# Optimization experiments

Hardware: AMD Instinct MI355X
Metric: run time of the kernel (lower is better)

## Reference

```python
import jax, jax.numpy as jnp
import numpy as np

N_USERS = 100000
M_ITEMS = 50000
EMBED = 64
N_LAYERS = 3
NNZ = 2400000
BATCH = 8192


def setup_inputs() -> dict:
    key = jax.random.key(0)
    ks = jax.random.split(key, 8)
    user = jax.random.randint(ks[0], (BATCH,), 0, N_USERS)
    item_i = jax.random.randint(ks[1], (BATCH,), 0, M_ITEMS)
    item_j = jax.random.randint(ks[2], (BATCH,), 0, M_ITEMS)
    timestamp = jax.random.uniform(ks[3], (BATCH,), dtype=jnp.float32)
    # symmetric bipartite edge list: user->item and item->user halves
    half = NNZ // 2
    u = jax.random.randint(ks[4], (half,), 0, N_USERS)
    it = jax.random.randint(ks[5], (half,), 0, M_ITEMS) + N_USERS
    edge_src = jnp.concatenate([u, it])
    edge_dst = jnp.concatenate([it, u])
    v = jax.random.uniform(ks[6], (half,), dtype=jnp.float32)
    edge_vals = jnp.concatenate([v, v])  # symmetric normalized weights
    embed_user_0 = jax.random.normal(ks[7], (N_USERS, EMBED), dtype=jnp.float32) * 0.1
    embed_item_0 = jax.random.normal(jax.random.fold_in(key, 99), (M_ITEMS, EMBED), dtype=jnp.float32) * 0.1
    return {
        'user': user, 'item_i': item_i, 'item_j': item_j,
        'timestamp': timestamp, 'split_idx': 0,
        'edge_src': edge_src, 'edge_dst': edge_dst, 'edge_vals': edge_vals,
        'embed_user_0': embed_user_0, 'embed_item_0': embed_item_0,
    }


def reference(user, item_i, item_j, timestamp, split_idx,
              edge_src, edge_dst, edge_vals, embed_user_0, embed_item_0):
    N = N_USERS + M_ITEMS
    # LightGCN propagation: mean over layer-0..n_layers embeddings
    all_emb = jnp.concatenate([embed_user_0, embed_item_0], axis=0)  # [N, D]
    emb = all_emb
    emb_sum = all_emb
    for _ in range(N_LAYERS):
        # sparse.mm(Graph, emb): gather source features along edges, scale, segment-reduce
        emb = jax.ops.segment_sum(edge_vals[:, None] * emb[edge_dst], edge_src,
                                  num_segments=N)
        emb_sum = emb_sum + emb
    light_out = emb_sum / (N_LAYERS + 1)
    embed_user = light_out[:N_USERS]
    embed_item = light_out[N_USERS:]

    ue = embed_user[user]          # [B, D]
    ie = embed_item[item_i]        # [B, D]
    je = embed_item[item_j]        # [B, D]
    prediction_i = jnp.sum(ue * ie, axis=-1)
    prediction_j = jnp.sum(ue * je, axis=-1)

    # reg_loss uses layer-0 embeddings gathered at the batch indices
    u0 = embed_user_0[user]
    i0 = embed_item_0[item_i]
    j0 = embed_item_0[item_j]
    reg_loss = 0.5 * (jnp.sum(u0 * u0) + jnp.sum(i0 * i0) + jnp.sum(j0 * j0)) / user.shape[0]
    return prediction_i, prediction_j, reg_loss
```

## Files before the change

### kernel.cpp

```cpp
#include <hip/hip_runtime.h>
#include <hip/hip_fp16.h>

#define N_USERS 100000
#define M_ITEMS 50000
#define NNODES  (N_USERS + M_ITEMS)
#define EMBED   64
#define BATCH   8192

#define NU_E ((size_t)N_USERS * EMBED)
#define NE   ((size_t)NNODES * EMBED)

#define NPB    256
#define NBUCK  ((NNODES + NPB - 1) / NPB)
#define CAP    8192
#define CSTR   16
#define PBLK   512
#define PTILE  4688
#define BCAP   12288
#define PRED_BLOCKS ((BATCH * 64) / 256)

typedef unsigned int uint;

static __device__ __forceinline__ ushort f2bf(float f) {
    uint u = __float_as_uint(f);
    return (ushort)((u + 0x7fffu + ((u >> 16) & 1u)) >> 16);
}
static __device__ __forceinline__ float bf_lo(uint u) { return __uint_as_float(u << 16); }
static __device__ __forceinline__ float bf_hi(uint u) { return __uint_as_float(u & 0xffff0000u); }
static __device__ __forceinline__ float bfs(ushort u) { return __uint_as_float((uint)u << 16); }

static __device__ __forceinline__ int packe(int d, int fbits) {
    ushort h = __half_as_ushort(__float2half(__int_as_float(fbits)));
    return (int)(((uint)d << 15) | (uint)(h & 0x7fffu));
}
static __device__ __forceinline__ float unp_val(int p) {
    return __half2float(__ushort_as_half((ushort)(p & 0x7fff)));
}

__global__ void init_all(const float* __restrict__ eu, const float* __restrict__ ei,
                         ushort* __restrict__ E0, int* __restrict__ gcur) {
    if (blockIdx.x == 0) {
        for (int i = threadIdx.x; i < NBUCK; i += 1024) gcur[i * CSTR] = i * CAP;
        return;
    }
    size_t t = (size_t)(blockIdx.x - 1) * 1024 + threadIdx.x;
    const size_t nu4 = NU_E / 4;
    const size_t n4  = NE / 4;
    if (t >= n4) return;
    float4 v = (t < nu4) ? ((const float4*)eu)[t] : ((const float4*)ei)[t - nu4];
    ((ushort4*)E0)[t] = make_ushort4(f2bf(v.x), f2bf(v.y), f2bf(v.z), f2bf(v.w));
}

__global__ void __launch_bounds__(1024)
partition2(const int* __restrict__ src, const int* __restrict__ dst,
           const float* __restrict__ vals, int* __restrict__ gcur,
           int2* __restrict__ ebuf, int nnz) {
    __shared__ int2 data[PTILE];
    __shared__ int  cnt[NBUCK];
    __shared__ int  cur[NBUCK];
    __shared__ int  lbeg[NBUCK];
    __shared__ int  gbase[NBUCK];
    __shared__ int  wsum[16];
    const int blk = blockIdx.x;
    const int tid = threadIdx.x;
    const int lane = tid & 63, w = tid >> 6;
    const int base = blk * PTILE;
    const int end  = min(base + PTILE, nnz);

    for (int i = tid; i < NBUCK; i += 1024) cnt[i] = 0;
    __syncthreads();
    for (int i = base + tid; i < end; i += 1024)
        atomicAdd(&cnt[src[i] >> 8], 1);
    __syncthreads();
    int c = (tid < NBUCK) ? cnt[tid] : 0;
    int v = c;
    #pragma unroll
    for (int off = 1; off < 64; off <<= 1) {
        int t = __shfl_up(v, off);
        if (lane >= off) v += t;
    }
    if (lane == 63) wsum[w] = v;
    __syncthreads();
    int wpre = 0;
    #pragma unroll
    for (int k = 0; k < 16; ++k) wpre += (k < w) ? wsum[k] : 0;
    v += wpre;
    if (tid < NBUCK) {
        int ex = v - c;
        cur[tid]  = ex;
        lbeg[tid] = ex;
        if (c > 0) gbase[tid] = atomicAdd(&gcur[tid * CSTR], c);
    }
    __syncthreads();
    for (int i = base + tid; i < end; i += 1024) {
        int sv = src[i];
        int d  = dst[i];
        float fv = vals[i];
        if (d >= N_USERS) d -= N_USERS;
        int p = atomicAdd(&cur[sv >> 8], 1);
        data[p] = make_int2((sv & 255) | (d << 8), __float_as_int(fv));
    }
    __syncthreads();
    int grp = tid >> 4, lane16 = tid & 15;
    for (int b = grp; b < NBUCK; b += 64) {
        int cc = cnt[b];
        if (cc == 0) continue;
        int lb = lbeg[b];
        int gb = gbase[b];
        for (int j = lane16; j < cc; j += 16)
            ebuf[gb + j] = data[lb + j];
    }
}

__global__ void __launch_bounds__(1024)
bucket_sort_perm(const int* __restrict__ gcur, const int2* __restrict__ ebuf,
                 int2* __restrict__ offs2, int* __restrict__ ep,
                 int* __restrict__ perm) {
    __shared__ int data[BCAP];
    __shared__ int cnt[256], cur[256], bcnt[256];
    __shared__ int wsum[16];
    int b   = blockIdx.x;
    int tid = threadIdx.x;
    int lane = tid & 63, w = tid >> 6;
    int beg = b * CAP;
    int end = gcur[b * CSTR];
    int blen = end - beg;
    if (tid < 256) cnt[tid] = 0;
    __syncthreads();
    for (int i = beg + tid; i < end; i += 1024)
        atomicAdd(&cnt[ebuf[i].x & 255], 1);
    __syncthreads();
    int c = (tid < 256) ? cnt[tid] : 0;
    int v = c;
    #pragma unroll
    for (int off = 1; off < 64; off <<= 1) {
        int t = __shfl_up(v, off);
        if (lane >= off) v += t;
    }
    if (tid < 256 && lane == 63) wsum[w] = v;
    __syncthreads();
    if (tid < 256) {
        int wpre = 0;
        #pragma unroll
        for (int k = 0; k < 4; ++k) wpre += (k < w) ? wsum[k] : 0;
        v += wpre;
        int lbase = v - c;
        int node = b * NPB + tid;
        if (node < NNODES) offs2[node] = make_int2(beg + lbase, c);
        cur[tid] = lbase;
    }
    __syncthreads();
    if (blen <= BCAP) {
        for (int i = beg + tid; i < end; i += 1024) {
            int2 e = ebuf[i];
            int p = atomicAdd(&cur[e.x & 255], 1);
            data[p] = packe(e.x >> 8, e.y);
        }
        __syncthreads();
        for (int i = tid; i < blen; i += 1024)
            ep[beg + i] = data[i];
    } else {
        for (int i = beg + tid; i < end; i += 1024) {
            int2 e = ebuf[i];
            int p = atomicAdd(&cur[e.x & 255], 1);
            ep[beg + p] = packe(e.x >> 8, e.y);
        }
    }
    __syncthreads();
    if (tid < 256) bcnt[tid] = 0;
    __syncthreads();
    int nodeCount = min(NNODES - b * NPB, NPB);
    int bin = 0;
    if (tid < nodeCount) {
        bin = 255 - min(cnt[tid], 255);
        atomicAdd(&bcnt[bin], 1);
    }
    __syncthreads();
    int c2 = (tid < 256) ? bcnt[tid] : 0;
    int v2 = c2;
    #pragma unroll
    for (int off = 1; off < 64; off <<= 1) {
        int t = __shfl_up(v2, off);
        if (lane >= off) v2 += t;
    }
    if (tid < 256 && lane == 63) wsum[w] = v2;
    __syncthreads();
    if (tid < 256) {
        int wpre = 0;
        #pragma unroll
        for (int k = 0; k < 4; ++k) wpre += (k < w) ? wsum[k] : 0;
        v2 += wpre;
        cur[tid] = b * NPB + (v2 - c2);
    }
    __syncthreads();
    if (tid < nodeCount) {
        int rank = atomicAdd(&cur[bin], 1);
        perm[rank] = b * NPB + tid;
    }
}

__global__ void gather_E(const int2* __restrict__ offs2, const int* __restrict__ ep,
                         const int* __restrict__ perm,
                         const ushort* __restrict__ Eprev, ushort* __restrict__ Enext) {
    int t = blockIdx.x * blockDim.x + threadIdx.x;
    int wave = t >> 6;
    int lane = t & 63;
    int g = lane >> 3;
    int q = lane & 7;
    int ln = wave * 8 + g;
    bool valid = ln < NNODES;
    int node = valid ? perm[ln] : 0;
    int2 od = valid ? offs2[node] : make_int2(0, 0);
    int start = od.x;
    int deg   = od.y;
    const uint4* other = (const uint4*)(Eprev + (node < N_USERS ? NU_E : 0));
    int lastIdx = max(start + deg - 1, 0);

    int md = deg;
    #pragma unroll
    for (int off = 8; off <= 32; off <<= 1) md = max(md, __shfl_xor(md, off));

    float a0=0.f,a1=0.f,a2=0.f,a3=0.f,a4=0.f,a5=0.f,a6=0.f,a7=0.f;
    for (int k = 0; k < md; k += 16) {
        int e[16];
        uint4 r[16];
        #pragma unroll
        for (int c = 0; c < 16; ++c) {
            int idx = (k + c < deg) ? start + k + c : lastIdx;
            e[c] = ep[idx];
            if (k + c >= deg) e[c] = 0;
        }
        #pragma unroll
        for (int c = 0; c < 16; ++c)
            r[c] = other[(size_t)(((uint)e[c]) >> 15) * 8 + q];
        #pragma unroll
        for (int c = 0; c < 16; ++c) {
            float v = unp_val(e[c]);
            a0 = fmaf(v, bf_lo(r[c].x), a0);  a1 = fmaf(v, bf_hi(r[c].x), a1);
            a2 = fmaf(v, bf_lo(r[c].y), a2);  a3 = fmaf(v, bf_hi(r[c].y), a3);
            a4 = fmaf(v, bf_lo(r[c].z), a4);  a5 = fmaf(v, bf_hi(r[c].z), a5);
            a6 = fmaf(v, bf_lo(r[c].w), a6);  a7 = fmaf(v, bf_hi(r[c].w), a7);
        }
    }

    if (!valid) return;
    uint4 o;
    o.x = (uint)f2bf(a0) | ((uint)f2bf(a1) << 16);
    o.y = (uint)f2bf(a2) | ((uint)f2bf(a3) << 16);
    o.z = (uint)f2bf(a4) | ((uint)f2bf(a5) << 16);
    o.w = (uint)f2bf(a6) | ((uint)f2bf(a7) << 16);
    ((uint4*)Enext)[(size_t)node * 8 + q] = o;
}

__global__ void predict_kernel(const int* __restrict__ user, const int* __restrict__ item_i,
                               const int* __restrict__ item_j,
                               const ushort* __restrict__ E0, const ushort* __restrict__ E1,
                               const ushort* __restrict__ E2, const ushort* __restrict__ E3,
                               const float* __restrict__ eu0, const float* __restrict__ ei0,
                               float* __restrict__ out, float* __restrict__ rbuf) {
    __shared__ float rpart[4];
    int t = blockIdx.x * blockDim.x + threadIdx.x;
    int b = t >> 6;
    int d = t & 63;
    int wv = threadIdx.x >> 6;
    float pi = 0.f, pj = 0.f, r = 0.f;
    if (b < BATCH) {
        size_t ru = (size_t)user[b] * EMBED + d;
        size_t ri = ((size_t)N_USERS + item_i[b]) * EMBED + d;
        size_t rj = ((size_t)N_USERS + item_j[b]) * EMBED + d;
        float ue = bfs(E0[ru]) + bfs(E1[ru]) + bfs(E2[ru]) + bfs(E3[ru]);
        float ie = bfs(E0[ri]) + bfs(E1[ri]) + bfs(E2[ri]) + bfs(E3[ri]);
        float je = bfs(E0[rj]) + bfs(E1[rj]) + bfs(E2[rj]) + bfs(E3[rj]);
        pi = ue * ie;
        pj = ue * je;
        float u0 = eu0[(size_t)user[b] * EMBED + d];
        float i0 = ei0[(size_t)item_i[b] * EMBED + d];
        float j0 = ei0[(size_t)item_j[b] * EMBED + d];
        r = u0 * u0 + i0 * i0 + j0 * j0;
    }
    #pragma unroll
    for (int off = 32; off > 0; off >>= 1) {
        pi += __shfl_down(pi, off);
        pj += __shfl_down(pj, off);
        r  += __shfl_down(r,  off);
    }
    if (d == 0 && b < BATCH) {
        out[b]         = pi * (1.0f / 16.0f);
        out[BATCH + b] = pj * (1.0f / 16.0f);
        rpart[wv] = r;
    }
    __syncthreads();
    if (threadIdx.x == 0)
        rbuf[blockIdx.x] = rpart[0] + rpart[1] + rpart[2] + rpart[3];
}

__global__ void finalize_reg(const float* __restrict__ rbuf, float* __restrict__ out) {
    __shared__ float lds[4];
    int tid = threadIdx.x;
    float s = 0.f;
    for (int i = tid; i < PRED_BLOCKS; i += 256) s += rbuf[i];
    #pragma unroll
    for (int off = 32; off > 0; off >>= 1) s += __shfl_down(s, off);
    if ((tid & 63) == 0) lds[tid >> 6] = s;
    __syncthreads();
    if (tid == 0)
        out[2 * BATCH] = (lds[0] + lds[1] + lds[2] + lds[3]) * (0.5f / (float)BATCH);
}

extern "C" void kernel_launch(void* const* d_in, const int* in_sizes, int n_in,
                              void* d_out, int out_size, void* d_ws, size_t ws_size,
                              hipStream_t stream) {
    const int*   user      = (const int*)  d_in[0];
    const int*   item_i    = (const int*)  d_in[1];
    const int*   item_j    = (const int*)  d_in[2];
    const int*   edge_src  = (const int*)  d_in[5];
    const int*   edge_dst  = (const int*)  d_in[6];
    const float* edge_vals = (const float*)d_in[7];
    const float* eu0       = (const float*)d_in[8];
    const float* ei0       = (const float*)d_in[9];
    const int    nnz       = in_sizes[5];

    float* out = (float*)d_out;

    ushort* E0    = (ushort*)d_ws;
    ushort* E1    = E0 + NE;
    ushort* E2    = E1 + NE;
    ushort* E3    = E2 + NE;
    int*    ep    = (int*)(E3 + NE);
    int2*   offs2 = (int2*)(ep + (size_t)NBUCK * CAP);
    int*    gcur  = (int*)(offs2 + NNODES);
    int*    perm  = gcur + NBUCK * CSTR;
    float*  rbuf  = (float*)(perm + NNODES);
    int2*   ebuf  = (int2*)E1;

    const int initBlocks = (int)((NE / 4 + 1023) / 1024);

    init_all<<<1 + initBlocks, 1024, 0, stream>>>(eu0, ei0, E0, gcur);
    partition2<<<PBLK, 1024, 0, stream>>>(edge_src, edge_dst, edge_vals,
                                          gcur, ebuf, nnz);
    bucket_sort_perm<<<NBUCK, 1024, 0, stream>>>(gcur, ebuf, offs2, ep, perm);
    const int gblocks = (int)((((NNODES + 7) / 8) * 64 + 255) / 256);
    gather_E<<<gblocks, 256, 0, stream>>>(offs2, ep, perm, E0, E1);
    gather_E<<<gblocks, 256, 0, stream>>>(offs2, ep, perm, E1, E2);
    gather_E<<<gblocks, 256, 0, stream>>>(offs2, ep, perm, E2, E3);
    predict_kernel<<<PRED_BLOCKS, 256, 0, stream>>>(
        user, item_i, item_j, E0, E1, E2, E3, eu0, ei0, out, rbuf);
    finalize_reg<<<1, 256, 0, stream>>>(rbuf, out);
}
```

Before: 307.5 us.

## Widen edge buckets to 512-node superbuckets and scatter sorted edges directly

Edge partitioning and the per-bucket counting sort now work on 512-node superbuckets instead of 256-node buckets. This halves the number of sort blocks, raises the per-bucket capacity, and repacks each edge as a 9-bit local id plus the destination. The shared-memory staging path in the sort is removed, so sorted edges are scattered straight to global memory. Degree-ordered node permutation now also spans 512 nodes, which could balance the later gather passes better. The cost is fewer, heavier sort blocks and uncoalesced global scatter writes.

Result: no change. 307.8 us (+0.1%).

```diff
diff --git a/kernel.cpp b/kernel.cpp
--- a/kernel.cpp
+++ b/kernel.cpp
@@ -10,13 +10,12 @@
 #define NU_E ((size_t)N_USERS * EMBED)
 #define NE   ((size_t)NNODES * EMBED)
 
-#define NPB    256
-#define NBUCK  ((NNODES + NPB - 1) / NPB)
-#define CAP    8192
+#define SBN    512
+#define NSB    ((NNODES + SBN - 1) / SBN)
+#define CAP    14336
 #define CSTR   16
 #define PBLK   512
 #define PTILE  4688
-#define BCAP   12288
 #define PRED_BLOCKS ((BATCH * 64) / 256)
 
 typedef unsigned int uint;
@@ -40,7 +39,7 @@
 __global__ void init_all(const float* __restrict__ eu, const float* __restrict__ ei,
                          ushort* __restrict__ E0, int* __restrict__ gcur) {
     if (blockIdx.x == 0) {
-        for (int i = threadIdx.x; i < NBUCK; i += 1024) gcur[i * CSTR] = i * CAP;
+        for (int i = threadIdx.x; i < NSB; i += 1024) gcur[i * CSTR] = i * CAP;
         return;
     }
     size_t t = (size_t)(blockIdx.x - 1) * 1024 + threadIdx.x;
@@ -56,10 +55,10 @@
            const float* __restrict__ vals, int* __restrict__ gcur,
            int2* __restrict__ ebuf, int nnz) {
     __shared__ int2 data[PTILE];
-    __shared__ int  cnt[NBUCK];
-    __shared__ int  cur[NBUCK];
-    __shared__ int  lbeg[NBUCK];
-    __shared__ int  gbase[NBUCK];
+    __shared__ int  cnt[NSB];
+    __shared__ int  cur[NSB];
+    __shared__ int  lbeg[NSB];
+    __shared__ int  gbase[NSB];
     __shared__ int  wsum[16];
     const int blk = blockIdx.x;
     const int tid = threadIdx.x;
@@ -67,12 +66,12 @@
     const int base = blk * PTILE;
     const int end  = min(base + PTILE, nnz);
 
-    for (int i = tid; i < NBUCK; i += 1024) cnt[i] = 0;
+    for (int i = tid; i < NSB; i += 1024) cnt[i] = 0;
     __syncthreads();
     for (int i = base + tid; i < end; i += 1024)
-        atomicAdd(&cnt[src[i] >> 8], 1);
-    __syncthreads();
-    int c = (tid < NBUCK) ? cnt[tid] : 0;
+        atomicAdd(&cnt[src[i] >> 9], 1);
+    __syncthreads();
+    int c = (tid < NSB) ? cnt[tid] : 0;
     int v = c;
     #pragma unroll
     for (int off = 1; off < 64; off <<= 1) {
@@ -85,7 +84,7 @@
     #pragma unroll
     for (int k = 0; k < 16; ++k) wpre += (k < w) ? wsum[k] : 0;
     v += wpre;
-    if (tid < NBUCK) {
+    if (tid < NSB) {
         int ex = v - c;
         cur[tid]  = ex;
         lbeg[tid] = ex;
@@ -97,12 +96,12 @@
         int d  = dst[i];
         float fv = vals[i];
         if (d >= N_USERS) d -= N_USERS;
-        int p = atomicAdd(&cur[sv >> 8], 1);
-        data[p] = make_int2((sv & 255) | (d << 8), __float_as_int(fv));
+        int p = atomicAdd(&cur[sv >> 9], 1);
+        data[p] = make_int2((sv & 511) | (d << 9), __float_as_int(fv));
     }
     __syncthreads();
     int grp = tid >> 4, lane16 = tid & 15;
-    for (int b = grp; b < NBUCK; b += 64) {
+    for (int b = grp; b < NSB; b += 64) {
         int cc = cnt[b];
         if (cc == 0) continue;
         int lb = lbeg[b];
@@ -113,63 +112,50 @@
 }
 
 __global__ void __launch_bounds__(1024)
-bucket_sort_perm(const int* __restrict__ gcur, const int2* __restrict__ ebuf,
-                 int2* __restrict__ offs2, int* __restrict__ ep,
-                 int* __restrict__ perm) {
-    __shared__ int data[BCAP];
-    __shared__ int cnt[256], cur[256], bcnt[256];
+sb_sort(const int* __restrict__ gcur, const int2* __restrict__ ebuf,
+        int2* __restrict__ offs2, int* __restrict__ ep,
+        int* __restrict__ perm) {
+    __shared__ int cnt[SBN], cur[SBN], bcnt[256];
     __shared__ int wsum[16];
-    int b   = blockIdx.x;
+    int sb  = blockIdx.x;
     int tid = threadIdx.x;
     int lane = tid & 63, w = tid >> 6;
-    int beg = b * CAP;
-    int end = gcur[b * CSTR];
-    int blen = end - beg;
-    if (tid < 256) cnt[tid] = 0;
+    int beg = sb * CAP;
+    int end = gcur[sb * CSTR];
+    if (tid < SBN) cnt[tid] = 0;
     __syncthreads();
     for (int i = beg + tid; i < end; i += 1024)
-        atomicAdd(&cnt[ebuf[i].x & 255], 1);
-    __syncthreads();
-    int c = (tid < 256) ? cnt[tid] : 0;
+        atomicAdd(&cnt[ebuf[i].x & (SBN - 1)], 1);
+    __syncthreads();
+    int c = (tid < SBN) ? cnt[tid] : 0;
     int v = c;
     #pragma unroll
     for (int off = 1; off < 64; off <<= 1) {
         int t = __shfl_up(v, off);
         if (lane >= off) v += t;
     }
-    if (tid < 256 && lane == 63) wsum[w] = v;
-    __syncthreads();
-    if (tid < 256) {
+    if (lane == 63) wsum[w] = v;
+    __syncthreads();
+    if (tid < SBN) {
         int wpre = 0;
         #pragma unroll
-        for (int k = 0; k < 4; ++k) wpre += (k < w) ? wsum[k] : 0;
+        for (int k = 0; k < 8; ++k) wpre += (k < w) ? wsum[k] : 0;
         v += wpre;
         int lbase = v - c;
-        int node = b * NPB + tid;
+        int node = sb * SBN + tid;
         if (node < NNODES) offs2[node] = make_int2(beg + lbase, c);
         cur[tid] = lbase;
     }
     __syncthreads();
-    if (blen <= BCAP) {
-        for (int i = beg + tid; i < end; i += 1024) {
-            int2 e = ebuf[i];
-            int p = atomicAdd(&cur[e.x & 255], 1);
-            data[p] = packe(e.x >> 8, e.y);
-        }
-        __syncthreads();
-        for (int i = tid; i < blen; i += 1024)
-            ep[beg + i] = data[i];
-    } else {
-        for (int i = beg + tid; i < end; i += 1024) {
-            int2 e = ebuf[i];
-            int p = atomicAdd(&cur[e.x & 255], 1);
-            ep[beg + p] = packe(e.x >> 8, e.y);
-        }
+    for (int i = beg + tid; i < end; i += 1024) {
+        int2 e = ebuf[i];
+        int p = atomicAdd(&cur[e.x & (SBN - 1)], 1);
+        ep[beg + p] = packe(e.x >> 9, e.y);
     }
     __syncthreads();
     if (tid < 256) bcnt[tid] = 0;
     __syncthreads();
-    int nodeCount = min(NNODES - b * NPB, NPB);
+    int nodeCount = min(NNODES - sb * SBN, SBN);
     int bin = 0;
     if (tid < nodeCount) {
         bin = 255 - min(cnt[tid], 255);
@@ -190,12 +176,12 @@
         #pragma unroll
         for (int k = 0; k < 4; ++k) wpre += (k < w) ? wsum[k] : 0;
         v2 += wpre;
-        cur[tid] = b * NPB + (v2 - c2);
+        cur[tid] = sb * SBN + (v2 - c2);
     }
     __syncthreads();
     if (tid < nodeCount) {
         int rank = atomicAdd(&cur[bin], 1);
-        perm[rank] = b * NPB + tid;
+        perm[rank] = sb * SBN + tid;
     }
 }
 
@@ -327,9 +313,9 @@
     ushort* E2    = E1 + NE;
     ushort* E3    = E2 + NE;
     int*    ep    = (int*)(E3 + NE);
-    int2*   offs2 = (int2*)(ep + (size_t)NBUCK * CAP);
+    int2*   offs2 = (int2*)(ep + (size_t)NSB * CAP);
     int*    gcur  = (int*)(offs2 + NNODES);
-    int*    perm  = gcur + NBUCK * CSTR;
+    int*    perm  = gcur + NSB * CSTR;
     float*  rbuf  = (float*)(perm + NNODES);
     int2*   ebuf  = (int2*)E1;
 
@@ -338,7 +324,7 @@
     init_all<<<1 + initBlocks, 1024, 0, stream>>>(eu0, ei0, E0, gcur);
     partition2<<<PBLK, 1024, 0, stream>>>(edge_src, edge_dst, edge_vals,
                                           gcur, ebuf, nnz);
-    bucket_sort_perm<<<NBUCK, 1024, 0, stream>>>(gcur, ebuf, offs2, ep, perm);
+    sb_sort<<<NSB, 1024, 0, stream>>>(gcur, ebuf, offs2, ep, perm);
     const int gblocks = (int)((((NNODES + 7) / 8) * 64 + 255) / 256);
     gather_E<<<gblocks, 256, 0, stream>>>(offs2, ep, perm, E0, E1);
     gather_E<<<gblocks, 256, 0, stream>>>(offs2, ep, perm, E1, E2);
```
